# Performance work log

Hardware: AMD Instinct MI355X
Metric: run time of the kernel (lower is better)

The kernel has to match this reference:

```python
import jax, jax.numpy as jnp
import numpy as np

E = 8        # num_sirens
F = 236      # siren_features (also per-expert output dim)
M = 441      # moe_features
C = 3        # input_size (coords)
OUT = 3      # output_size
HL = 3       # layersiren - 2 hidden sine layers
W0 = 30.0
N = 65536


def setup_inputs() -> dict:
    key = jax.random.key(0)
    ks = jax.random.split(key, 20)
    u = lambda k, shape, lim: jax.random.uniform(k, shape, jnp.float32, -lim, lim)
    sl = lambda fan_in: float(np.sqrt(6.0 / fan_in) / 30.0)  # sine_init limit
    inp = {}
    inp["x"] = jax.random.uniform(ks[0], (N, C), jnp.float32, -1.0, 1.0)
    # SIREN experts, stacked over E. First layer: first_layer_sine_init (1/fan_in).
    inp["siren_W1"] = u(ks[1], (E, C, F), 1.0 / C)
    inp["siren_b1"] = u(ks[2], (E, F), 1.0 / C)
    inp["siren_Wh"] = u(ks[3], (HL, E, F, F), sl(F))
    inp["siren_bh"] = u(ks[4], (HL, E, F), sl(F))
    inp["siren_Wo"] = u(ks[5], (E, F, F), sl(F))
    inp["siren_bo"] = u(ks[6], (E, F), sl(F))
    # Gating MLP (Moe): Linear(3,M)+ReLU, Linear(M,M)+ReLU, Linear(M,E)+Top1+Softmax
    inp["moe_W1"] = u(ks[7], (C, M), sl(C))
    inp["moe_b1"] = u(ks[8], (M,), sl(C))
    inp["moe_W2"] = u(ks[9], (M, M), sl(M))
    inp["moe_b2"] = u(ks[10], (M,), sl(M))
    inp["moe_W3"] = u(ks[11], (M, E), sl(M))
    inp["moe_b3"] = u(ks[12], (E,), sl(M))
    # Decoder: Linear(E*F, F)+ReLU, Linear(F, OUT)
    inp["dec_W1"] = u(ks[13], (E * F, F), sl(E * F))
    inp["dec_b1"] = u(ks[14], (F,), sl(E * F))
    inp["dec_W2"] = u(ks[15], (F, OUT), sl(F))
    inp["dec_b2"] = u(ks[16], (OUT,), sl(F))
    return inp


def reference(x, siren_W1, siren_b1, siren_Wh, siren_bh, siren_Wo, siren_bo,
              moe_W1, moe_b1, moe_W2, moe_b2, moe_W3, moe_b3,
              dec_W1, dec_b1, dec_W2, dec_b2):
    n = x.shape[0]
    # --- parallel SIREN experts, batched over E ---
    h = jnp.sin(W0 * (jnp.einsum('nc,ecf->enf', x, siren_W1) + siren_b1[:, None, :]))
    for i in range(HL):  # fixed small layer loop
        h = jnp.sin(W0 * (jnp.einsum('enf,efg->eng', h, siren_Wh[i]) + siren_bh[i][:, None, :]))
    so = jnp.einsum('enf,efg->eng', h, siren_Wo) + siren_bo[:, None, :]       # (E,N,F)
    siren_cat = jnp.transpose(so, (1, 0, 2)).reshape(n, E * F)                # cat along -1, expert-major
    # --- gating MLP + Top-1 + softmax ---
    g = jax.nn.relu(x @ moe_W1 + moe_b1)
    g = jax.nn.relu(g @ moe_W2 + moe_b2)
    logits = g @ moe_W3 + moe_b3                                              # (N,E)
    _, top_idx = jax.lax.top_k(logits, 1)
    mask = jnp.zeros_like(logits).at[jnp.arange(n)[:, None], top_idx].set(1.0)
    masked = jnp.where(mask > 0, logits, -jnp.inf)
    weights = jax.nn.softmax(masked, axis=-1)                                 # one-hot at argmax
    # --- KL(uniform || weights), batchmean (stored as self.kl_loss in torch) ---
    logw = jnp.log(weights + 1e-10)
    unif = jnp.asarray(1.0 / E, logw.dtype)
    kl = jnp.sum(unif * (jnp.log(unif) - logw)) / n
    # --- repeat_interleave(F) * concat, then decoder ---
    w_full = jnp.broadcast_to(weights[:, :, None], (n, E, F)).reshape(n, E * F)
    dec_in = w_full * siren_cat
    out = jax.nn.relu(dec_in @ dec_W1 + dec_b1) @ dec_W2 + dec_b2             # (N,OUT)
    return out, kl
```

## Files before the change

kernel.cpp:

```cpp
#include <hip/hip_runtime.h>
#include <cstdint>

typedef unsigned short ushort_t;
typedef short bf16x8 __attribute__((ext_vector_type(8)));
typedef unsigned short u16x8 __attribute__((ext_vector_type(8)));
typedef float f32x4 __attribute__((ext_vector_type(4)));

#define NPTS 65536
#define WS_CNT 0
#define WS_BKT 64
#define OFF_W2S 1048640
#define OFF_W3T 1450048
#define OFF_SWT 1464640
#define OFF_D2F 6379840
#define WS_FAST 6388032u
#define WS_SLOW (64 + 8 * NPTS * 2)

__device__ __forceinline__ float bf2f(ushort_t u) {
  union { unsigned u; float f; } c; c.u = ((unsigned)u) << 16; return c.f;
}
__device__ __forceinline__ ushort_t f2bf(float f) {
  union { float f; unsigned u; } c; c.f = f;
  unsigned u = c.u + 0x7fffu + ((c.u >> 16) & 1u);
  return (ushort_t)(u >> 16);
}
__device__ __forceinline__ float rbf(float v) { return bf2f(f2bf(v)); }
__device__ __forceinline__ bool nan_bits(float v) {
  union { float f; unsigned u; } c; c.f = v;
  return ((c.u >> 23) & 0xFFu) == 0xFFu && (c.u & 0x7FFFFFu) != 0u;
}

__global__ void k_sentinel(float* out) {
  if (threadIdx.x == 0) out[0] = 1.0e30f;
}


__global__ __launch_bounds__(256) void k_prep_fast(
    const float* __restrict__ sWh, const float* __restrict__ sWo,
    const float* __restrict__ dW1, const float* __restrict__ mW2,
    const float* __restrict__ mW3, const float* __restrict__ dW2,
    int* __restrict__ counts, ushort_t* __restrict__ W2S,
    ushort_t* __restrict__ w3T, ushort_t* __restrict__ swt,
    ushort_t* __restrict__ d2f, float* __restrict__ out)
{
  long gid = (long)blockIdx.x * 256 + threadIdx.x;
  long gs = (long)gridDim.x * 256;
  for (long i = gid; i < 307200; i += gs) {
    int mat = (int)(i / 7680);
    int r = (int)(i - (long)mat * 7680);
    int t = r >> 9;
    int r2 = r & 511;
    int kt = r2 >> 6, lane = r2 & 63;
    int n = t * 16 + (lane & 15);
    int q = lane >> 4;
    const float* W = (mat < 24) ? (sWh + (long)mat * 55696)
                   : (mat < 32) ? (sWo + (long)(mat - 24) * 55696)
                                : (dW1 + (long)(mat - 32) * 55696);
    u16x8 tv;
    #pragma unroll
    for (int u = 0; u < 8; ++u) {
      int k = kt * 32 + q * 8 + u;
      tv[u] = (n < 236 && k < 236) ? f2bf(W[k * 236 + n]) : (ushort_t)0;
    }
    *(u16x8*)(swt + i * 8) = tv;
  }
  for (long i = gid; i < 4096; i += gs) {
    int u = (int)(i & 7), lane = (int)((i >> 3) & 63), kt = (int)(i >> 9);
    int n = lane & 15, k = kt * 32 + ((lane >> 4) << 3) + u;
    d2f[i] = (n < 3 && k < 236) ? f2bf(dW2[k * 3 + n]) : (ushort_t)0;
  }
  for (long i = gid; i < 25088; i += gs) {
    int kt = (int)(i / (28 * 64));
    int rem = (int)(i - (long)kt * 28 * 64);
    int nt = rem / 64, lane = rem - nt * 64;
    int l15 = lane & 15, quad = lane >> 4;
    int n = nt * 16 + l15;
    u16x8 tv;
    #pragma unroll
    for (int u = 0; u < 8; ++u) {
      int k = kt * 32 + quad * 8 + u;
      tv[u] = (k < 441 && n < 441) ? f2bf(mW2[(long)k * 441 + n]) : (ushort_t)0;
    }
    *(u16x8*)(W2S + i * 8) = tv;
  }
  for (long i = gid; i < 7296; i += gs) {
    int e = (int)(i / 456), c = (int)(i - (long)e * 456);
    w3T[i] = (e < 8 && c < 441) ? f2bf(mW3[(long)c * 8 + e]) : (ushort_t)0;
  }
  if (gid < 8) counts[gid] = 0;
  if (gid == 8) out[NPTS * 3] = 18.125f;
}

__global__ __launch_bounds__(256) void k_gate_fast(
    const float* __restrict__ x,
    const float* __restrict__ mW1, const float* __restrict__ mb1,
    const float* __restrict__ mb2, const float* __restrict__ mb3,
    const ushort_t* __restrict__ W2S, const ushort_t* __restrict__ w3Tg,
    int* __restrict__ counts, ushort_t* __restrict__ bucket)
{
  __shared__ ushort_t At[64][40];
  __shared__ float W1c[1792];
  __shared__ float xl[192];
  __shared__ ushort_t chunkC[64][72];
  __shared__ ushort_t w3T[16][456];
  __shared__ float b2c[448];
  __shared__ unsigned char bexp[64];

  int tid = threadIdx.x;
  int blk = blockIdx.x;
  if (tid < 192) {
    int p = tid / 3, c = tid - p * 3;
    xl[tid] = rbf(x[(blk * 64 + p) * 3 + c]);
  }
  for (int j = tid; j < 1792; j += 256) {
    int c = j / 448, m = j - c * 448;
    float v = 0.f;
    if (m < 441) v = (c < 3) ? rbf(mW1[c * 441 + m]) : rbf(mb1[m]);
    W1c[j] = v;
  }
  for (int j = tid; j < 448; j += 256) b2c[j] = (j < 441) ? rbf(mb2[j]) : 0.f;
  for (int ch = tid; ch < 912; ch += 256)
    *(u16x8*)(&w3T[0][0] + ch * 8) = *(const u16x8*)(w3Tg + ch * 8);

  int w = tid >> 6, lane = tid & 63;
  int l15 = lane & 15, quad = lane >> 4;

  f32x4 acc[4][7];
  #pragma unroll
  for (int a = 0; a < 4; ++a)
    #pragma unroll
    for (int b = 0; b < 7; ++b)
      acc[a][b] = (f32x4){0.f, 0.f, 0.f, 0.f};

  int am = tid >> 2, ak = (tid & 3) * 8;

  for (int kt = 0; kt < 14; ++kt) {
    int kk0 = kt * 32;
    __syncthreads();
    {
      float x0 = xl[am * 3], x1 = xl[am * 3 + 1], x2 = xl[am * 3 + 2];
      u16x8 tmp;
      #pragma unroll
      for (int u = 0; u < 8; ++u) {
        int j = kk0 + ak + u;
        ushort_t h = 0;
        if (j < 441) {
          float t = x0 * W1c[j];
          t = fmaf(x1, W1c[448 + j], t);
          t = fmaf(x2, W1c[896 + j], t);
          t = rbf(t);
          t = rbf(t + W1c[1344 + j]);
          t = fmaxf(t, 0.f);
          h = f2bf(t);
        }
        tmp[u] = h;
      }
      *(u16x8*)(At[am] + ak) = tmp;
    }
    __syncthreads();
    bf16x8 bfr[7];
    #pragma unroll
    for (int j = 0; j < 7; ++j)
      bfr[j] = *(const bf16x8*)(W2S + ((kt * 28 + (w + 4 * j)) * 64 + lane) * 8);
    #pragma unroll
    for (int mt = 0; mt < 4; ++mt) {
      bf16x8 a = *(const bf16x8*)(&At[mt * 16 + l15][quad * 8]);
      #pragma unroll
      for (int j = 0; j < 7; ++j)
        acc[mt][j] = __builtin_amdgcn_mfma_f32_16x16x32_bf16(a, bfr[j], acc[mt][j], 0, 0, 0);
    }
  }

  f32x4 acc3[4];
  #pragma unroll
  for (int mt = 0; mt < 4; ++mt) acc3[mt] = (f32x4){0.f, 0.f, 0.f, 0.f};
  #pragma unroll
  for (int j = 0; j < 7; ++j) {
    __syncthreads();
    #pragma unroll
    for (int mt = 0; mt < 4; ++mt) {
      #pragma unroll
      for (int r = 0; r < 4; ++r) {
        int cg = j * 64 + w * 16 + l15;
        int m = mt * 16 + quad * 4 + r;
        float v = rbf(acc[mt][j][r]);
        v = rbf(v + b2c[cg]);
        v = fmaxf(v, 0.f);
        chunkC[m][w * 16 + l15] = f2bf(v);
      }
    }
    __syncthreads();
    bf16x8 b0 = *(const bf16x8*)(&w3T[l15][j * 64 + quad * 8]);
    bf16x8 b1 = *(const bf16x8*)(&w3T[l15][j * 64 + 32 + quad * 8]);
    #pragma unroll
    for (int mt = 0; mt < 4; ++mt) {
      bf16x8 a0 = *(const bf16x8*)(&chunkC[mt * 16 + l15][quad * 8]);
      bf16x8 a1 = *(const bf16x8*)(&chunkC[mt * 16 + l15][32 + quad * 8]);
      acc3[mt] = __builtin_amdgcn_mfma_f32_16x16x32_bf16(a0, b0, acc3[mt], 0, 0, 0);
      acc3[mt] = __builtin_amdgcn_mfma_f32_16x16x32_bf16(a1, b1, acc3[mt], 0, 0, 0);
    }
  }
  float b3v = (l15 < 8) ? rbf(mb3[l15]) : 0.f;
  if (w == 0) {
    #pragma unroll
    for (int mt = 0; mt < 4; ++mt) {
      #pragma unroll
      for (int r = 0; r < 4; ++r) {
        float lv = rbf(acc3[mt][r]);
        lv = rbf(lv + b3v);
        float v = (l15 < 8) ? lv : -1.0e30f;
        int ii = l15;
        #pragma unroll
        for (int mk = 1; mk < 8; mk <<= 1) {
          float ov = __shfl_xor(v, mk);
          int oi = __shfl_xor(ii, mk);
          if (ov > v || (ov == v && oi < ii)) { v = ov; ii = oi; }
        }
        if (l15 == 0) bexp[mt * 16 + quad * 4 + r] = (unsigned char)ii;
      }
    }
  }
  __syncthreads();
  if (tid < 64) {
    int bi = (int)bexp[tid];
    int slot = 0;
    #pragma unroll
    for (int ee = 0; ee < 8; ++ee) {
      unsigned long long msk = __ballot(bi == ee);
      if (bi == ee) {
        int leader = (int)__builtin_ctzll(msk);
        int rank = __popcll(msk & ((1ull << tid) - 1ull));
        int basep = 0;
        if (tid == leader) basep = atomicAdd(&counts[ee], __popcll(msk));
        basep = __shfl(basep, leader);
        slot = basep + rank;
      }
    }
    bucket[bi * NPTS + slot] = (ushort_t)(blk * 64 + tid);
  }
}

__global__ __launch_bounds__(256) void k_sdec_fast(
    const float* __restrict__ x,
    const float* __restrict__ sW1, const float* __restrict__ sb1,
    const float* __restrict__ sbh, const float* __restrict__ sbo,
    const float* __restrict__ db1, const float* __restrict__ db2,
    const ushort_t* __restrict__ swt, const ushort_t* __restrict__ d2f,
    const int* __restrict__ counts, const ushort_t* __restrict__ bucket,
    float* __restrict__ out)
{
  __shared__ ushort_t hA[64][264];
  __shared__ int idxl[64];
  __shared__ float xl[64][3];
  __shared__ float wc[944];

  int b = blockIdx.x;
  int e = -1, base = 0, cnte = 0, cum = 0;
  #pragma unroll
  for (int ee = 0; ee < 8; ++ee) {
    int c = counts[ee];
    int nb = (c + 63) >> 6;
    if (e < 0 && b < cum + nb) { e = ee; base = (b - cum) << 6; cnte = c; }
    cum += nb;
  }
  if (e < 0) return;
  int np = min(64, cnte - base);
  int tid = threadIdx.x;

  if (tid < 64) {
    int s = base + (tid < np ? tid : 0);
    idxl[tid] = (int)bucket[e * NPTS + s];
  }
  __syncthreads();
  if (tid < 192) {
    int p = tid / 3, c = tid - p * 3;
    xl[p][c] = rbf(x[idxl[p] * 3 + c]);
  }
  for (int j = tid; j < 944; j += 256)
    wc[j] = (j < 708) ? rbf(sW1[e * 708 + j]) : 30.f * rbf(sb1[e * 236 + (j - 708)]);
  __syncthreads();

  int w = tid >> 6, lane = tid & 63;
  int l15 = lane & 15, quad = lane >> 4;

  for (int i = lane; i < 16 * 264; i += 64) {
    int pr = i / 264, f = i - pr * 264;
    int p = w * 16 + pr;
    ushort_t hv = 0;
    if (f < 236) {
      float v = xl[p][0] * wc[f];
      v = fmaf(xl[p][1], wc[236 + f], v);
      v = fmaf(xl[p][2], wc[472 + f], v);
      v = fmaf(30.f, v, wc[708 + f]);
      hv = f2bf(__sinf(v));
    }
    hA[p][f] = hv;
  }
  __syncthreads();

  for (int l = 0; l < 5; ++l) {
    const ushort_t* Wt; const float* bias; int act;
    if (l < 3)       { Wt = swt + (l * 8 + e) * 61440; bias = sbh + (l * 8 + e) * 236; act = 0; }
    else if (l == 3) { Wt = swt + (24 + e) * 61440;    bias = sbo + e * 236;           act = 1; }
    else             { Wt = swt + (32 + e) * 61440;    bias = db1;                     act = 2; }

    bf16x8 afr[4][8];
    #pragma unroll
    for (int mt = 0; mt < 4; ++mt)
      #pragma unroll
      for (int kt = 0; kt < 8; ++kt)
        afr[mt][kt] = *(const bf16x8*)(&hA[mt * 16 + l15][kt * 32 + quad * 8]);
    __syncthreads();

    #pragma unroll
    for (int tt = 0; tt < 4; ++tt) {
      int t = w + tt * 4;
      if (t < 15) {
        f32x4 acc[4];
        #pragma unroll
        for (int mt = 0; mt < 4; ++mt) acc[mt] = (f32x4){0.f, 0.f, 0.f, 0.f};
        #pragma unroll
        for (int kt = 0; kt < 8; ++kt) {
          bf16x8 bb = *(const bf16x8*)(Wt + ((t * 8 + kt) * 64 + lane) * 8);
          #pragma unroll
          for (int mt = 0; mt < 4; ++mt)
            acc[mt] = __builtin_amdgcn_mfma_f32_16x16x32_bf16(afr[mt][kt], bb, acc[mt], 0, 0, 0);
        }
        int n = t * 16 + l15;
        if (n < 236) {
          float bv = rbf(bias[n]);
          float b30 = 30.f * bv;
          #pragma unroll
          for (int mt = 0; mt < 4; ++mt) {
            #pragma unroll
            for (int r = 0; r < 4; ++r) {
              int m = mt * 16 + quad * 4 + r;
              float v;
              if (act == 0)      v = __sinf(fmaf(30.f, acc[mt][r], b30));
              else if (act == 1) v = acc[mt][r] + bv;
              else               v = fmaxf(acc[mt][r] + bv, 0.f);
              hA[m][n] = f2bf(v);
            }
          }
        }
      }
    }
    __syncthreads();
  }

  {
    f32x4 acc = (f32x4){0.f, 0.f, 0.f, 0.f};
    #pragma unroll
    for (int kt = 0; kt < 8; ++kt) {
      bf16x8 a = *(const bf16x8*)(&hA[w * 16 + l15][kt * 32 + quad * 8]);
      bf16x8 bb = *(const bf16x8*)(d2f + (kt * 64 + lane) * 8);
      acc = __builtin_amdgcn_mfma_f32_16x16x32_bf16(a, bb, acc, 0, 0, 0);
    }
    if (l15 < 3) {
      float bv = rbf(db2[l15]);
      #pragma unroll
      for (int r = 0; r < 4; ++r) {
        int p = w * 16 + quad * 4 + r;
        if (p < np) {
          float s = acc[r] + bv;
          out[idxl[p] * 3 + l15] = nan_bits(s) ? 16.0f : fminf(fmaxf(s, -4.f), 4.f);
        }
      }
    }
  }
}


__global__ void k_prep_slow(int* counts, float* out) {
  int t = threadIdx.x;
  if (t < 8) counts[t] = 0;
  if (t == 8) out[NPTS * 3] = 18.125f;
}

__global__ __launch_bounds__(256) void k_gate_slow(
    const float* __restrict__ x,
    const float* __restrict__ mW1, const float* __restrict__ mb1,
    const float* __restrict__ mW2, const float* __restrict__ mb2,
    const float* __restrict__ mW3, const float* __restrict__ mb3,
    int* __restrict__ counts, ushort_t* __restrict__ bucket)
{
  extern __shared__ char smem[];
  ushort_t* At  = (ushort_t*)smem;
  ushort_t* Bt  = (ushort_t*)(smem + 5120);
  float*    W1c = (float*)(smem + 40960);
  ushort_t* g2  = (ushort_t*)smem;
  float*    b2c = (float*)(smem + 58368);
  float*    xl  = (float*)(smem + 60160);
  float*    lg  = (float*)(smem + 60928);

  int tid = threadIdx.x;
  int blk = blockIdx.x;
  if (tid < 192) {
    int p = tid / 3, c = tid - p * 3;
    xl[tid] = rbf(x[(blk * 64 + p) * 3 + c]);
  }
  for (int j = tid; j < 1792; j += 256) {
    int c = j / 448, m = j - c * 448;
    float v = 0.f;
    if (m < 441) v = (c < 3) ? rbf(mW1[c * 441 + m]) : rbf(mb1[m]);
    W1c[j] = v;
  }
  for (int j = tid; j < 448; j += 256) b2c[j] = (j < 441) ? rbf(mb2[j]) : 0.f;

  int w = tid >> 6, lane = tid & 63;
  int l15 = lane & 15, quad = lane >> 4;

  f32x4 acc[4][7];
  #pragma unroll
  for (int a = 0; a < 4; ++a)
    #pragma unroll
    for (int b = 0; b < 7; ++b)
      acc[a][b] = (f32x4){0.f, 0.f, 0.f, 0.f};

  int am = tid >> 2, ak = (tid & 3) * 8;

  for (int kt = 0; kt < 14; ++kt) {
    int kk0 = kt * 32;
    __syncthreads();
    {
      float x0 = xl[am * 3], x1 = xl[am * 3 + 1], x2 = xl[am * 3 + 2];
      u16x8 tmp;
      #pragma unroll
      for (int u = 0; u < 8; ++u) {
        int j = kk0 + ak + u;
        ushort_t h = 0;
        if (j < 441) {
          float t = x0 * W1c[j];
          t = fmaf(x1, W1c[448 + j], t);
          t = fmaf(x2, W1c[896 + j], t);
          t = rbf(t);
          t = rbf(t + W1c[1344 + j]);
          t = fmaxf(t, 0.f);
          h = f2bf(t);
        }
        tmp[u] = h;
      }
      *(u16x8*)(At + am * 40 + ak) = tmp;
    }
    {
      int n1 = tid;
      #pragma unroll
      for (int q = 0; q < 4; ++q) {
        u16x8 tv;
        #pragma unroll
        for (int u = 0; u < 8; ++u) {
          int kk = kk0 + q * 8 + u;
          tv[u] = (kk < 441 && n1 < 441) ? f2bf(mW2[kk * 441 + n1]) : (ushort_t)0;
        }
        *(u16x8*)(Bt + n1 * 40 + q * 8) = tv;
      }
      int n2 = tid + 256;
      if (n2 < 448) {
        #pragma unroll
        for (int q = 0; q < 4; ++q) {
          u16x8 tv;
          #pragma unroll
          for (int u = 0; u < 8; ++u) {
            int kk = kk0 + q * 8 + u;
            tv[u] = (kk < 441 && n2 < 441) ? f2bf(mW2[kk * 441 + n2]) : (ushort_t)0;
          }
          *(u16x8*)(Bt + n2 * 40 + q * 8) = tv;
        }
      }
    }
    __syncthreads();
    bf16x8 bfr[7];
    #pragma unroll
    for (int j = 0; j < 7; ++j) {
      int nt = w + 4 * j;
      bfr[j] = *(const bf16x8*)(Bt + (nt * 16 + l15) * 40 + quad * 8);
    }
    #pragma unroll
    for (int mt = 0; mt < 4; ++mt) {
      bf16x8 a = *(const bf16x8*)(At + (mt * 16 + l15) * 40 + quad * 8);
      #pragma unroll
      for (int j = 0; j < 7; ++j)
        acc[mt][j] = __builtin_amdgcn_mfma_f32_16x16x32_bf16(a, bfr[j], acc[mt][j], 0, 0, 0);
    }
  }
  __syncthreads();
  #pragma unroll
  for (int mt = 0; mt < 4; ++mt) {
    #pragma unroll
    for (int j = 0; j < 7; ++j) {
      int c = (w + 4 * j) * 16 + l15;
      float bv = b2c[c];
      #pragma unroll
      for (int r = 0; r < 4; ++r) {
        int m = mt * 16 + quad * 4 + r;
        float v = rbf(acc[mt][j][r]);
        v = rbf(v + bv);
        v = fmaxf(v, 0.f);
        g2[m * 456 + c] = f2bf(v);
      }
    }
  }
  __syncthreads();
  {
    int m3 = tid >> 2, eg = tid & 3;
    float s0 = 0.f, s1 = 0.f;
    const ushort_t* row = g2 + m3 * 456;
    for (int j = 0; j < 441; ++j) {
      float gv = bf2f(row[j]);
      s0 = fmaf(gv, rbf(mW3[j * 8 + 2 * eg]), s0);
      s1 = fmaf(gv, rbf(mW3[j * 8 + 2 * eg + 1]), s1);
    }
    s0 = rbf(rbf(s0) + rbf(mb3[2 * eg]));
    s1 = rbf(rbf(s1) + rbf(mb3[2 * eg + 1]));
    lg[m3 * 8 + 2 * eg] = s0;
    lg[m3 * 8 + 2 * eg + 1] = s1;
  }
  __syncthreads();
  if (tid < 64) {
    float best = lg[tid * 8];
    int bi = 0;
    #pragma unroll
    for (int e = 1; e < 8; ++e) {
      float v = lg[tid * 8 + e];
      if (v > best) { best = v; bi = e; }
    }
    int slot = 0;
    #pragma unroll
    for (int e = 0; e < 8; ++e) {
      unsigned long long msk = __ballot(bi == e);
      if (bi == e) {
        int leader = (int)__builtin_ctzll(msk);
        int rank = __popcll(msk & ((1ull << tid) - 1ull));
        int basep = 0;
        if (tid == leader) basep = atomicAdd(&counts[e], __popcll(msk));
        basep = __shfl(basep, leader);
        slot = basep + rank;
      }
    }
    bucket[bi * NPTS + slot] = (ushort_t)(blk * 64 + tid);
  }
}

__global__ __launch_bounds__(256) void k_sdec_slow(
    const float* __restrict__ x,
    const float* __restrict__ sW1, const float* __restrict__ sb1,
    const float* __restrict__ sWh, const float* __restrict__ sbh,
    const float* __restrict__ sWo, const float* __restrict__ sbo,
    const float* __restrict__ dW1, const float* __restrict__ db1,
    const float* __restrict__ dW2, const float* __restrict__ db2,
    const int* __restrict__ counts, const ushort_t* __restrict__ bucket,
    float* __restrict__ out)
{
  __shared__ ushort_t hA[64][264];
  __shared__ ushort_t wb[2][16][264];
  __shared__ int idxl[64];
  __shared__ float xl[64][3];
  __shared__ float wc[944];

  int e = blockIdx.y;
  int base = blockIdx.x * 64;
  int cnt = counts[e];
  if (base >= cnt) return;
  int np = min(64, cnt - base);
  int tid = threadIdx.x;

  if (tid < 64) {
    int s = base + (tid < np ? tid : 0);
    idxl[tid] = (int)bucket[e * NPTS + s];
  }
  __syncthreads();
  if (tid < 192) {
    int p = tid / 3, c = tid - p * 3;
    xl[p][c] = rbf(x[idxl[p] * 3 + c]);
  }
  for (int j = tid; j < 944; j += 256)
    wc[j] = (j < 708) ? rbf(sW1[e * 708 + j]) : rbf(sb1[e * 236 + (j - 708)]);
  for (int t = tid; t < 64 * 28; t += 256) {
    int p = t / 28, cc = 236 + (t - p * 28);
    hA[p][cc] = 0;
  }
  __syncthreads();
  for (int t = tid; t < 64 * 236; t += 256) {
    int p = t / 236, f = t - p * 236;
    float v = xl[p][0] * wc[f];
    v = fmaf(xl[p][1], wc[236 + f], v);
    v = fmaf(xl[p][2], wc[472 + f], v);
    v = rbf(v);
    v = rbf(v + wc[708 + f]);
    v = rbf(30.f * v);
    hA[p][f] = f2bf(sinf(v));
  }

  int w = tid >> 6, lane = tid & 63;
  int l15 = lane & 15, quad = lane >> 4;

  auto stage = [&](const float* W, int t, ushort_t (*buf)[264]) {
    int k = tid;
    if (k < 236) {
      const float* srcW = W + k * 236 + t * 16;
      int jmax = 236 - t * 16; if (jmax > 16) jmax = 16;
      float tv[16];
      if (jmax == 16) {
        *(f32x4*)(tv)      = *(const f32x4*)(srcW);
        *(f32x4*)(tv + 4)  = *(const f32x4*)(srcW + 4);
        *(f32x4*)(tv + 8)  = *(const f32x4*)(srcW + 8);
        *(f32x4*)(tv + 12) = *(const f32x4*)(srcW + 12);
      } else {
        *(f32x4*)(tv)      = *(const f32x4*)(srcW);
        *(f32x4*)(tv + 4)  = *(const f32x4*)(srcW + 4);
        *(f32x4*)(tv + 8)  = *(const f32x4*)(srcW + 8);
        tv[12] = tv[13] = tv[14] = tv[15] = 0.f;
      }
      #pragma unroll
      for (int j = 0; j < 16; ++j)
        buf[j][k] = (j < jmax) ? f2bf(tv[j]) : (ushort_t)0;
    } else {
      #pragma unroll
      for (int j = 0; j < 16; ++j) buf[j][k] = 0;
    }
  };

  for (int l = 0; l < 5; ++l) {
    const float* W; const float* bias; int act;
    if (l < 3)       { W = sWh + (l * 8 + e) * 55696; bias = sbh + (l * 8 + e) * 236; act = 0; }
    else if (l == 3) { W = sWo + e * 55696;           bias = sbo + e * 236;           act = 1; }
    else             { W = dW1 + e * 55696;           bias = db1;                     act = 2; }

    __syncthreads();
    bf16x8 afr[4][8];
    #pragma unroll
    for (int mt = 0; mt < 4; ++mt)
      #pragma unroll
      for (int kt = 0; kt < 8; ++kt)
        afr[mt][kt] = *(const bf16x8*)(&hA[mt * 16 + l15][kt * 32 + quad * 8]);
    stage(W, 0, wb[0]);
    __syncthreads();

    for (int t = 0; t < 15; ++t) {
      if (t < 14) stage(W, t + 1, wb[(t + 1) & 1]);
      if ((t & 3) == w) {
        f32x4 acc[4];
        #pragma unroll
        for (int mt = 0; mt < 4; ++mt) acc[mt] = (f32x4){0.f, 0.f, 0.f, 0.f};
        #pragma unroll
        for (int kt = 0; kt < 8; ++kt) {
          bf16x8 b = *(const bf16x8*)(&wb[t & 1][l15][kt * 32 + quad * 8]);
          #pragma unroll
          for (int mt = 0; mt < 4; ++mt)
            acc[mt] = __builtin_amdgcn_mfma_f32_16x16x32_bf16(afr[mt][kt], b, acc[mt], 0, 0, 0);
        }
        int n = t * 16 + l15;
        if (n < 236) {
          float bv = rbf(bias[n]);
          #pragma unroll
          for (int mt = 0; mt < 4; ++mt) {
            #pragma unroll
            for (int r = 0; r < 4; ++r) {
              int m = mt * 16 + quad * 4 + r;
              float v = rbf(acc[mt][r]);
              v = rbf(v + bv);
              if (act == 0) { v = rbf(30.f * v); v = sinf(v); }
              else if (act == 2) v = fmaxf(v, 0.f);
              hA[m][n] = f2bf(v);
            }
          }
        }
      }
      __syncthreads();
    }
  }

  for (int j = tid; j < 711; j += 256)
    wc[j] = (j < 708) ? rbf(dW2[j]) : rbf(db2[j - 708]);
  __syncthreads();
  if (tid < 192) {
    int p = tid / 3, o = tid - p * 3;
    if (p < np) {
      float s = 0.f;
      for (int k = 0; k < 236; ++k)
        s = fmaf(bf2f(hA[p][k]), wc[k * 3 + o], s);
      s = rbf(s);
      s = rbf(s + wc[708 + o]);
      out[idxl[p] * 3 + o] = nan_bits(s) ? 16.0f : fminf(fmaxf(s, -4.f), 4.f);
    }
  }
}

extern "C" void kernel_launch(void* const* d_in, const int* in_sizes, int n_in,
                              void* d_out, int out_size, void* d_ws, size_t ws_size,
                              hipStream_t stream) {
  const float* x   = (const float*)d_in[0];
  const float* sW1 = (const float*)d_in[1];
  const float* sb1 = (const float*)d_in[2];
  const float* sWh = (const float*)d_in[3];
  const float* sbh = (const float*)d_in[4];
  const float* sWo = (const float*)d_in[5];
  const float* sbo = (const float*)d_in[6];
  const float* mW1 = (const float*)d_in[7];
  const float* mb1 = (const float*)d_in[8];
  const float* mW2 = (const float*)d_in[9];
  const float* mb2 = (const float*)d_in[10];
  const float* mW3 = (const float*)d_in[11];
  const float* mb3 = (const float*)d_in[12];
  const float* dW1 = (const float*)d_in[13];
  const float* db1 = (const float*)d_in[14];
  const float* dW2 = (const float*)d_in[15];
  const float* db2 = (const float*)d_in[16];

  float* outp = (float*)d_out;
  char* ws = (char*)d_ws;
  int* counts      = (int*)(ws + WS_CNT);
  ushort_t* bucket = (ushort_t*)(ws + WS_BKT);

  if (ws_size >= (size_t)WS_FAST) {
    ushort_t* W2S = (ushort_t*)(ws + OFF_W2S);
    ushort_t* w3T = (ushort_t*)(ws + OFF_W3T);
    ushort_t* swt = (ushort_t*)(ws + OFF_SWT);
    ushort_t* d2f = (ushort_t*)(ws + OFF_D2F);
    k_prep_fast<<<dim3(2048), dim3(256), 0, stream>>>(sWh, sWo, dW1, mW2, mW3, dW2,
                                                      counts, W2S, w3T, swt, d2f, outp);
    k_gate_fast<<<dim3(1024), dim3(256), 0, stream>>>(x, mW1, mb1, mb2, mb3,
                                                      W2S, w3T, counts, bucket);
    k_sdec_fast<<<dim3(1032), dim3(256), 0, stream>>>(x, sW1, sb1, sbh, sbo,
                                                      db1, db2, swt, d2f,
                                                      counts, bucket, outp);
  } else if (ws_size >= (size_t)WS_SLOW) {
    k_prep_slow<<<dim3(1), dim3(64), 0, stream>>>(counts, outp);
    k_gate_slow<<<dim3(1024), dim3(256), 62976, stream>>>(x, mW1, mb1, mW2, mb2, mW3, mb3,
                                                          counts, bucket);
    k_sdec_slow<<<dim3(1024, 8), dim3(256), 0, stream>>>(x, sW1, sb1, sWh, sbh, sWo, sbo,
                                                         dW1, db1, dW2, db2, counts, bucket, outp);
  } else {
    k_sentinel<<<dim3(1), dim3(64), 0, stream>>>(outp);
  }
}
```

Measured before the change: 281.7 us.

## Precompute full gating layer-1 activations in LDS and drop per-k-tile barriers

The gate kernel now computes the whole 64x441 ReLU first-layer activation tile into shared memory once, before the MFMA loop, so the 14-step K loop runs without the two __syncthreads per iteration. To fit in LDS, the W1/b1/b2 caches are stored as bf16, and the chunkC and w3T buffers alias the At region after the main loop. This cuts barriers and interleaved ALU/MFMA stalls, but LDS use per block rises (about 58KB for At), which may lower occupancy. The scalar activation stores into At with a 456 stride may also cause bank conflicts.

```diff
diff --git a/kernel.cpp b/kernel.cpp
--- a/kernel.cpp
+++ b/kernel.cpp
@@ -98,13 +98,13 @@
     const ushort_t* __restrict__ W2S, const ushort_t* __restrict__ w3Tg,
     int* __restrict__ counts, ushort_t* __restrict__ bucket)
 {
-  __shared__ ushort_t At[64][40];
-  __shared__ float W1c[1792];
+  __shared__ ushort_t At[64][456];
   __shared__ float xl[192];
-  __shared__ ushort_t chunkC[64][72];
-  __shared__ ushort_t w3T[16][456];
-  __shared__ float b2c[448];
+  __shared__ ushort_t W1c[1792];
+  __shared__ ushort_t b2c[448];
   __shared__ unsigned char bexp[64];
+  ushort_t (*chunkC)[72] = (ushort_t (*)[72])(&At[0][0]);
+  ushort_t (*w3T)[456]   = (ushort_t (*)[456])(&At[0][0] + 4608);
 
   int tid = threadIdx.x;
   int blk = blockIdx.x;
@@ -114,13 +114,27 @@
   }
   for (int j = tid; j < 1792; j += 256) {
     int c = j / 448, m = j - c * 448;
-    float v = 0.f;
-    if (m < 441) v = (c < 3) ? rbf(mW1[c * 441 + m]) : rbf(mb1[m]);
+    ushort_t v = 0;
+    if (m < 441) v = (c < 3) ? f2bf(mW1[c * 441 + m]) : f2bf(mb1[m]);
     W1c[j] = v;
   }
-  for (int j = tid; j < 448; j += 256) b2c[j] = (j < 441) ? rbf(mb2[j]) : 0.f;
-  for (int ch = tid; ch < 912; ch += 256)
-    *(u16x8*)(&w3T[0][0] + ch * 8) = *(const u16x8*)(w3Tg + ch * 8);
+  for (int j = tid; j < 448; j += 256) b2c[j] = (j < 441) ? f2bf(mb2[j]) : (ushort_t)0;
+  __syncthreads();
+  for (int t = tid; t < 64 * 448; t += 256) {
+    int p = t / 448, j = t - p * 448;
+    ushort_t h = 0;
+    if (j < 441) {
+      float v = xl[p * 3] * bf2f(W1c[j]);
+      v = fmaf(xl[p * 3 + 1], bf2f(W1c[448 + j]), v);
+      v = fmaf(xl[p * 3 + 2], bf2f(W1c[896 + j]), v);
+      v = rbf(v);
+      v = rbf(v + bf2f(W1c[1344 + j]));
+      v = fmaxf(v, 0.f);
+      h = f2bf(v);
+    }
+    At[p][j] = h;
+  }
+  __syncthreads();
 
   int w = tid >> 6, lane = tid & 63;
   int l15 = lane & 15, quad = lane >> 4;
@@ -132,44 +146,23 @@
     for (int b = 0; b < 7; ++b)
       acc[a][b] = (f32x4){0.f, 0.f, 0.f, 0.f};
 
-  int am = tid >> 2, ak = (tid & 3) * 8;
-
   for (int kt = 0; kt < 14; ++kt) {
-    int kk0 = kt * 32;
-    __syncthreads();
-    {
-      float x0 = xl[am * 3], x1 = xl[am * 3 + 1], x2 = xl[am * 3 + 2];
-      u16x8 tmp;
-      #pragma unroll
-      for (int u = 0; u < 8; ++u) {
-        int j = kk0 + ak + u;
-        ushort_t h = 0;
-        if (j < 441) {
-          float t = x0 * W1c[j];
-          t = fmaf(x1, W1c[448 + j], t);
-          t = fmaf(x2, W1c[896 + j], t);
-          t = rbf(t);
-          t = rbf(t + W1c[1344 + j]);
-          t = fmaxf(t, 0.f);
-          h = f2bf(t);
-        }
-        tmp[u] = h;
-      }
-      *(u16x8*)(At[am] + ak) = tmp;
-    }
-    __syncthreads();
     bf16x8 bfr[7];
     #pragma unroll
     for (int j = 0; j < 7; ++j)
       bfr[j] = *(const bf16x8*)(W2S + ((kt * 28 + (w + 4 * j)) * 64 + lane) * 8);
     #pragma unroll
     for (int mt = 0; mt < 4; ++mt) {
-      bf16x8 a = *(const bf16x8*)(&At[mt * 16 + l15][quad * 8]);
+      bf16x8 a = *(const bf16x8*)(&At[mt * 16 + l15][kt * 32 + quad * 8]);
       #pragma unroll
       for (int j = 0; j < 7; ++j)
         acc[mt][j] = __builtin_amdgcn_mfma_f32_16x16x32_bf16(a, bfr[j], acc[mt][j], 0, 0, 0);
     }
   }
+
+  __syncthreads();
+  for (int ch = tid; ch < 912; ch += 256)
+    *(u16x8*)((ushort_t*)w3T + ch * 8) = *(const u16x8*)(w3Tg + ch * 8);
 
   f32x4 acc3[4];
   #pragma unroll
@@ -184,7 +177,7 @@
         int cg = j * 64 + w * 16 + l15;
         int m = mt * 16 + quad * 4 + r;
         float v = rbf(acc[mt][j][r]);
-        v = rbf(v + b2c[cg]);
+        v = rbf(v + bf2f(b2c[cg]));
         v = fmaxf(v, 0.f);
         chunkC[m][w * 16 + l15] = f2bf(v);
       }
```

Measured after the change: 348.6 us. +23.7%, slower.

## Fuse prep, gating and expert/decoder kernels into one persistent kernel with grid barriers

Applied to the files above, without the earlier changes.

Replaces three kernel launches (weight prep, gating/bucketing, SIREN+decoder) with a single 1024-block kernel that uses atomic-counter grid barriers between phases. Shared memory is carved from one buffer and reused across phases, and counters are zeroed with a memset before launch. The goal is to remove launch gaps and tail effects between stages. The risks are deadlock if not all 1024 blocks are co-resident, barrier spin cost, and a tighter launch bound that may limit registers for the accumulator-heavy gating phase.

```diff
diff --git a/kernel.cpp b/kernel.cpp
--- a/kernel.cpp
+++ b/kernel.cpp
@@ -8,6 +8,7 @@
 
 #define NPTS 65536
 #define WS_CNT 0
+#define WS_BAR 32
 #define WS_BKT 64
 #define OFF_W2S 1048640
 #define OFF_W3T 1450048
@@ -15,6 +16,7 @@
 #define OFF_D2F 6379840
 #define WS_FAST 6388032u
 #define WS_SLOW (64 + 8 * NPTS * 2)
+#define NB_FUSED 1024
 
 __device__ __forceinline__ float bf2f(ushort_t u) {
   union { unsigned u; float f; } c; c.u = ((unsigned)u) << 16; return c.f;
@@ -34,336 +36,342 @@
   if (threadIdx.x == 0) out[0] = 1.0e30f;
 }
 
-
-__global__ __launch_bounds__(256) void k_prep_fast(
-    const float* __restrict__ sWh, const float* __restrict__ sWo,
-    const float* __restrict__ dW1, const float* __restrict__ mW2,
-    const float* __restrict__ mW3, const float* __restrict__ dW2,
-    int* __restrict__ counts, ushort_t* __restrict__ W2S,
-    ushort_t* __restrict__ w3T, ushort_t* __restrict__ swt,
-    ushort_t* __restrict__ d2f, float* __restrict__ out)
+__device__ __forceinline__ void grid_barrier(int* bar) {
+  __syncthreads();
+  if (threadIdx.x == 0) {
+    __threadfence();
+    atomicAdd(bar, 1);
+    while (atomicAdd(bar, 0) < NB_FUSED) { __builtin_amdgcn_s_sleep(2); }
+    __threadfence();
+  }
+  __syncthreads();
+}
+
+__global__ __launch_bounds__(256, 4) void k_fused(
+    const float* __restrict__ x,
+    const float* __restrict__ sW1, const float* __restrict__ sb1,
+    const float* __restrict__ sWh, const float* __restrict__ sbh,
+    const float* __restrict__ sWo, const float* __restrict__ sbo,
+    const float* __restrict__ mW1, const float* __restrict__ mb1,
+    const float* __restrict__ mW2, const float* __restrict__ mb2,
+    const float* __restrict__ mW3, const float* __restrict__ mb3,
+    const float* __restrict__ dW1, const float* __restrict__ db1,
+    const float* __restrict__ dW2, const float* __restrict__ db2,
+    int* __restrict__ counts, int* __restrict__ bars,
+    ushort_t* __restrict__ bucket,
+    ushort_t* __restrict__ W2S, ushort_t* __restrict__ w3Tg,
+    ushort_t* __restrict__ swt, ushort_t* __restrict__ d2f,
+    float* __restrict__ out)
 {
-  long gid = (long)blockIdx.x * 256 + threadIdx.x;
-  long gs = (long)gridDim.x * 256;
-  for (long i = gid; i < 307200; i += gs) {
-    int mat = (int)(i / 7680);
-    int r = (int)(i - (long)mat * 7680);
-    int t = r >> 9;
-    int r2 = r & 511;
-    int kt = r2 >> 6, lane = r2 & 63;
-    int n = t * 16 + (lane & 15);
-    int q = lane >> 4;
-    const float* W = (mat < 24) ? (sWh + (long)mat * 55696)
-                   : (mat < 32) ? (sWo + (long)(mat - 24) * 55696)
-                                : (dW1 + (long)(mat - 32) * 55696);
-    u16x8 tv;
-    #pragma unroll
-    for (int u = 0; u < 8; ++u) {
-      int k = kt * 32 + q * 8 + u;
-      tv[u] = (n < 236 && k < 236) ? f2bf(W[k * 236 + n]) : (ushort_t)0;
-    }
-    *(u16x8*)(swt + i * 8) = tv;
-  }
-  for (long i = gid; i < 4096; i += gs) {
-    int u = (int)(i & 7), lane = (int)((i >> 3) & 63), kt = (int)(i >> 9);
-    int n = lane & 15, k = kt * 32 + ((lane >> 4) << 3) + u;
-    d2f[i] = (n < 3 && k < 236) ? f2bf(dW2[k * 3 + n]) : (ushort_t)0;
-  }
-  for (long i = gid; i < 25088; i += gs) {
-    int kt = (int)(i / (28 * 64));
-    int rem = (int)(i - (long)kt * 28 * 64);
-    int nt = rem / 64, lane = rem - nt * 64;
-    int l15 = lane & 15, quad = lane >> 4;
-    int n = nt * 16 + l15;
-    u16x8 tv;
-    #pragma unroll
-    for (int u = 0; u < 8; ++u) {
-      int k = kt * 32 + quad * 8 + u;
-      tv[u] = (k < 441 && n < 441) ? f2bf(mW2[(long)k * 441 + n]) : (ushort_t)0;
-    }
-    *(u16x8*)(W2S + i * 8) = tv;
-  }
-  for (long i = gid; i < 7296; i += gs) {
-    int e = (int)(i / 456), c = (int)(i - (long)e * 456);
-    w3T[i] = (e < 8 && c < 441) ? f2bf(mW3[(long)c * 8 + e]) : (ushort_t)0;
-  }
-  if (gid < 8) counts[gid] = 0;
-  if (gid == 8) out[NPTS * 3] = 18.125f;
-}
-
-__global__ __launch_bounds__(256) void k_gate_fast(
-    const float* __restrict__ x,
-    const float* __restrict__ mW1, const float* __restrict__ mb1,
-    const float* __restrict__ mb2, const float* __restrict__ mb3,
-    const ushort_t* __restrict__ W2S, const ushort_t* __restrict__ w3Tg,
-    int* __restrict__ counts, ushort_t* __restrict__ bucket)
-{
-  __shared__ ushort_t At[64][40];
-  __shared__ float W1c[1792];
-  __shared__ float xl[192];
-  __shared__ ushort_t chunkC[64][72];
-  __shared__ ushort_t w3T[16][456];
-  __shared__ float b2c[448];
-  __shared__ unsigned char bexp[64];
-
+  __shared__ __align__(16) char smem[38720];
   int tid = threadIdx.x;
   int blk = blockIdx.x;
-  if (tid < 192) {
-    int p = tid / 3, c = tid - p * 3;
-    xl[tid] = rbf(x[(blk * 64 + p) * 3 + c]);
-  }
-  for (int j = tid; j < 1792; j += 256) {
-    int c = j / 448, m = j - c * 448;
-    float v = 0.f;
-    if (m < 441) v = (c < 3) ? rbf(mW1[c * 441 + m]) : rbf(mb1[m]);
-    W1c[j] = v;
-  }
-  for (int j = tid; j < 448; j += 256) b2c[j] = (j < 441) ? rbf(mb2[j]) : 0.f;
-  for (int ch = tid; ch < 912; ch += 256)
-    *(u16x8*)(&w3T[0][0] + ch * 8) = *(const u16x8*)(w3Tg + ch * 8);
-
   int w = tid >> 6, lane = tid & 63;
   int l15 = lane & 15, quad = lane >> 4;
 
-  f32x4 acc[4][7];
-  #pragma unroll
-  for (int a = 0; a < 4; ++a)
-    #pragma unroll
-    for (int b = 0; b < 7; ++b)
-      acc[a][b] = (f32x4){0.f, 0.f, 0.f, 0.f};
-
-  int am = tid >> 2, ak = (tid & 3) * 8;
-
-  for (int kt = 0; kt < 14; ++kt) {
-    int kk0 = kt * 32;
+  {
+    long gid = (long)blk * 256 + tid;
+    const long gs = (long)NB_FUSED * 256;
+    for (long i = gid; i < 307200; i += gs) {
+      int mat = (int)(i / 7680);
+      int r = (int)(i - (long)mat * 7680);
+      int t = r >> 9;
+      int r2 = r & 511;
+      int kt = r2 >> 6, ln = r2 & 63;
+      int n = t * 16 + (ln & 15);
+      int q = ln >> 4;
+      const float* W = (mat < 24) ? (sWh + (long)mat * 55696)
+                     : (mat < 32) ? (sWo + (long)(mat - 24) * 55696)
+                                  : (dW1 + (long)(mat - 32) * 55696);
+      u16x8 tv;
+      #pragma unroll
+      for (int u = 0; u < 8; ++u) {
+        int k = kt * 32 + q * 8 + u;
+        tv[u] = (n < 236 && k < 236) ? f2bf(W[k * 236 + n]) : (ushort_t)0;
+      }
+      *(u16x8*)(swt + i * 8) = tv;
+    }
+    for (long i = gid; i < 4096; i += gs) {
+      int u = (int)(i & 7), ln = (int)((i >> 3) & 63), kt = (int)(i >> 9);
+      int n = ln & 15, k = kt * 32 + ((ln >> 4) << 3) + u;
+      d2f[i] = (n < 3 && k < 236) ? f2bf(dW2[k * 3 + n]) : (ushort_t)0;
+    }
+    for (long i = gid; i < 25088; i += gs) {
+      int kt = (int)(i / (28 * 64));
+      int rem = (int)(i - (long)kt * 28 * 64);
+      int nt = rem / 64, ln = rem - nt * 64;
+      int n = nt * 16 + (ln & 15);
+      int q = ln >> 4;
+      u16x8 tv;
+      #pragma unroll
+      for (int u = 0; u < 8; ++u) {
+        int k = kt * 32 + q * 8 + u;
+        tv[u] = (k < 441 && n < 441) ? f2bf(mW2[(long)k * 441 + n]) : (ushort_t)0;
+      }
+      *(u16x8*)(W2S + i * 8) = tv;
+    }
+    for (long i = gid; i < 7296; i += gs) {
+      int e = (int)(i / 456), c = (int)(i - (long)e * 456);
+      w3Tg[i] = (e < 8 && c < 441) ? f2bf(mW3[(long)c * 8 + e]) : (ushort_t)0;
+    }
+    if (gid == 0) out[NPTS * 3] = 18.125f;
+  }
+  grid_barrier(&bars[0]);
+
+  {
+    ushort_t (*At)[40]     = (ushort_t (*)[40])(smem);
+    float*    W1c          = (float*)(smem + 5120);
+    float*    xl           = (float*)(smem + 12288);
+    ushort_t (*chunkC)[72] = (ushort_t (*)[72])(smem + 13056);
+    ushort_t (*w3T)[456]   = (ushort_t (*)[456])(smem + 22272);
+    float*    b2c          = (float*)(smem + 36864);
+    unsigned char* bexp    = (unsigned char*)(smem + 38656);
+
+    if (tid < 192) {
+      int p = tid / 3, c = tid - p * 3;
+      xl[tid] = rbf(x[(blk * 64 + p) * 3 + c]);
+    }
+    for (int j = tid; j < 1792; j += 256) {
+      int c = j / 448, m = j - c * 448;
+      float v = 0.f;
+      if (m < 441) v = (c < 3) ? rbf(mW1[c * 441 + m]) : rbf(mb1[m]);
+      W1c[j] = v;
+    }
+    for (int j = tid; j < 448; j += 256) b2c[j] = (j < 441) ? rbf(mb2[j]) : 0.f;
+    for (int ch = tid; ch < 912; ch += 256)
+      *(u16x8*)(&w3T[0][0] + ch * 8) = *(const u16x8*)(w3Tg + ch * 8);
+
+    f32x4 acc[4][7];
+    #pragma unroll
+    for (int a = 0; a < 4; ++a)
+      #pragma unroll
+      for (int b = 0; b < 7; ++b)
+        acc[a][b] = (f32x4){0.f, 0.f, 0.f, 0.f};
+
+    int am = tid >> 2, ak = (tid & 3) * 8;
+
+    for (int kt = 0; kt < 14; ++kt) {
+      int kk0 = kt * 32;
+      __syncthreads();
+      {
+        float x0 = xl[am * 3], x1 = xl[am * 3 + 1], x2 = xl[am * 3 + 2];
+        u16x8 tmp;
+        #pragma unroll
+        for (int u = 0; u < 8; ++u) {
+          int j = kk0 + ak + u;
+          ushort_t h = 0;
+          if (j < 441) {
+            float t = x0 * W1c[j];
+            t = fmaf(x1, W1c[448 + j], t);
+            t = fmaf(x2, W1c[896 + j], t);
+            t = rbf(t);
+            t = rbf(t + W1c[1344 + j]);
+            t = fmaxf(t, 0.f);
+            h = f2bf(t);
+          }
+          tmp[u] = h;
+        }
+        *(u16x8*)(At[am] + ak) = tmp;
+      }
+      __syncthreads();
+      bf16x8 bfr[7];
+      #pragma unroll
+      for (int j = 0; j < 7; ++j)
+        bfr[j] = *(const bf16x8*)(W2S + ((kt * 28 + (w + 4 * j)) * 64 + lane) * 8);
+      #pragma unroll
+      for (int mt = 0; mt < 4; ++mt) {
+        bf16x8 a = *(const bf16x8*)(&At[mt * 16 + l15][quad * 8]);
+        #pragma unroll
+        for (int j = 0; j < 7; ++j)
+          acc[mt][j] = __builtin_amdgcn_mfma_f32_16x16x32_bf16(a, bfr[j], acc[mt][j], 0, 0, 0);
+      }
+    }
+
+    f32x4 acc3[4];
+    #pragma unroll
+    for (int mt = 0; mt < 4; ++mt) acc3[mt] = (f32x4){0.f, 0.f, 0.f, 0.f};
+    #pragma unroll
+    for (int j = 0; j < 7; ++j) {
+      __syncthreads();
+      #pragma unroll
+      for (int mt = 0; mt < 4; ++mt) {
+        #pragma unroll
+        for (int r = 0; r < 4; ++r) {
+          int cg = j * 64 + w * 16 + l15;
+          int m = mt * 16 + quad * 4 + r;
+          float v = rbf(acc[mt][j][r]);
+          v = rbf(v + b2c[cg]);
+          v = fmaxf(v, 0.f);
+          chunkC[m][w * 16 + l15] = f2bf(v);
+        }
+      }
+      __syncthreads();
+      bf16x8 b0 = *(const bf16x8*)(&w3T[l15][j * 64 + quad * 8]);
+      bf16x8 b1 = *(const bf16x8*)(&w3T[l15][j * 64 + 32 + quad * 8]);
+      #pragma unroll
+      for (int mt = 0; mt < 4; ++mt) {
+        bf16x8 a0 = *(const bf16x8*)(&chunkC[mt * 16 + l15][quad * 8]);
+        bf16x8 a1 = *(const bf16x8*)(&chunkC[mt * 16 + l15][32 + quad * 8]);
+        acc3[mt] = __builtin_amdgcn_mfma_f32_16x16x32_bf16(a0, b0, acc3[mt], 0, 0, 0);
+        acc3[mt] = __builtin_amdgcn_mfma_f32_16x16x32_bf16(a1, b1, acc3[mt], 0, 0, 0);
+      }
+    }
+    float b3v = (l15 < 8) ? rbf(mb3[l15]) : 0.f;
+    if (w == 0) {
+      #pragma unroll
+      for (int mt = 0; mt < 4; ++mt) {
+        #pragma unroll
+        for (int r = 0; r < 4; ++r) {
+          float lv = rbf(acc3[mt][r]);
+          lv = rbf(lv + b3v);
+          float v = (l15 < 8) ? lv : -1.0e30f;
+          int ii = l15;
+          #pragma unroll
+          for (int mk = 1; mk < 8; mk <<= 1) {
+            float ov = __shfl_xor(v, mk);
+            int oi = __shfl_xor(ii, mk);
+            if (ov > v || (ov == v && oi < ii)) { v = ov; ii = oi; }
+          }
+          if (l15 == 0) bexp[mt * 16 + quad * 4 + r] = (unsigned char)ii;
+        }
+      }
+    }
     __syncthreads();
-    {
-      float x0 = xl[am * 3], x1 = xl[am * 3 + 1], x2 = xl[am * 3 + 2];
-      u16x8 tmp;
-      #pragma unroll
-      for (int u = 0; u < 8; ++u) {
-        int j = kk0 + ak + u;
-        ushort_t h = 0;
-        if (j < 441) {
-          float t = x0 * W1c[j];
-          t = fmaf(x1, W1c[448 + j], t);
-          t = fmaf(x2, W1c[896 + j], t);
-          t = rbf(t);
-          t = rbf(t + W1c[1344 + j]);
-          t = fmaxf(t, 0.f);
-          h = f2bf(t);
-        }
-        tmp[u] = h;
-      }
-      *(u16x8*)(At[am] + ak) = tmp;
-    }
-    __syncthreads();
-    bf16x8 bfr[7];
-    #pragma unroll
-    for (int j = 0; j < 7; ++j)
-      bfr[j] = *(const bf16x8*)(W2S + ((kt * 28 + (w + 4 * j)) * 64 + lane) * 8);
-    #pragma unroll
-    for (int mt = 0; mt < 4; ++mt) {
-      bf16x8 a = *(const bf16x8*)(&At[mt * 16 + l15][quad * 8]);
-      #pragma unroll
-      for (int j = 0; j < 7; ++j)
-        acc[mt][j] = __builtin_amdgcn_mfma_f32_16x16x32_bf16(a, bfr[j], acc[mt][j], 0, 0, 0);
-    }
-  }
-
-  f32x4 acc3[4];
-  #pragma unroll
-  for (int mt = 0; mt < 4; ++mt) acc3[mt] = (f32x4){0.f, 0.f, 0.f, 0.f};
-  #pragma unroll
-  for (int j = 0; j < 7; ++j) {
-    __syncthreads();
-    #pragma unroll
-    for (int mt = 0; mt < 4; ++mt) {
-      #pragma unroll
-      for (int r = 0; r < 4; ++r) {
-        int cg = j * 64 + w * 16 + l15;
-        int m = mt * 16 + quad * 4 + r;
-        float v = rbf(acc[mt][j][r]);
-        v = rbf(v + b2c[cg]);
-        v = fmaxf(v, 0.f);
-        chunkC[m][w * 16 + l15] = f2bf(v);
-      }
-    }
-    __syncthreads();
-    bf16x8 b0 = *(const bf16x8*)(&w3T[l15][j * 64 + quad * 8]);
-    bf16x8 b1 = *(const bf16x8*)(&w3T[l15][j * 64 + 32 + quad * 8]);
-    #pragma unroll
-    for (int mt = 0; mt < 4; ++mt) {
-      bf16x8 a0 = *(const bf16x8*)(&chunkC[mt * 16 + l15][quad * 8]);
-      bf16x8 a1 = *(const bf16x8*)(&chunkC[mt * 16 + l15][32 + quad * 8]);
-      acc3[mt] = __builtin_amdgcn_mfma_f32_16x16x32_bf16(a0, b0, acc3[mt], 0, 0, 0);
-      acc3[mt] = __builtin_amdgcn_mfma_f32_16x16x32_bf16(a1, b1, acc3[mt], 0, 0, 0);
-    }
-  }
-  float b3v = (l15 < 8) ? rbf(mb3[l15]) : 0.f;
-  if (w == 0) {
-    #pragma unroll
-    for (int mt = 0; mt < 4; ++mt) {
-      #pragma unroll
-      for (int r = 0; r < 4; ++r) {
-        float lv = rbf(acc3[mt][r]);
-        lv = rbf(lv + b3v);
-        float v = (l15 < 8) ? lv : -1.0e30f;
-        int ii = l15;
-        #pragma unroll
-        for (int mk = 1; mk < 8; mk <<= 1) {
-          float ov = __shfl_xor(v, mk);
-          int oi = __shfl_xor(ii, mk);
-          if (ov > v || (ov == v && oi < ii)) { v = ov; ii = oi; }
-        }
-        if (l15 == 0) bexp[mt * 16 + quad * 4 + r] = (unsigned char)ii;
-      }
-    }
-  }
-  __syncthreads();
-  if (tid < 64) {
-    int bi = (int)bexp[tid];
-    int slot = 0;
-    #pragma unroll
-    for (int ee = 0; ee < 8; ++ee) {
-      unsigned long long msk = __ballot(bi == ee);
-      if (bi == ee) {
-        int leader = (int)__builtin_ctzll(msk);
-        int rank = __popcll(msk & ((1ull << tid) - 1ull));
-        int basep = 0;
-        if (tid == leader) basep = atomicAdd(&counts[ee], __popcll(msk));
-        basep = __shfl(basep, leader);
-        slot = basep + rank;
-      }
-    }
-    bucket[bi * NPTS + slot] = (ushort_t)(blk * 64 + tid);
-  }
-}
-
-__global__ __launch_bounds__(256) void k_sdec_fast(
-    const float* __restrict__ x,
-    const float* __restrict__ sW1, const float* __restrict__ sb1,
-    const float* __restrict__ sbh, const float* __restrict__ sbo,
-    const float* __restrict__ db1, const float* __restrict__ db2,
-    const ushort_t* __restrict__ swt, const ushort_t* __restrict__ d2f,
-    const int* __restrict__ counts, const ushort_t* __restrict__ bucket,
-    float* __restrict__ out)
-{
-  __shared__ ushort_t hA[64][264];
-  __shared__ int idxl[64];
-  __shared__ float xl[64][3];
-  __shared__ float wc[944];
-
-  int b = blockIdx.x;
-  int e = -1, base = 0, cnte = 0, cum = 0;
-  #pragma unroll
-  for (int ee = 0; ee < 8; ++ee) {
-    int c = counts[ee];
-    int nb = (c + 63) >> 6;
-    if (e < 0 && b < cum + nb) { e = ee; base = (b - cum) << 6; cnte = c; }
-    cum += nb;
-  }
-  if (e < 0) return;
-  int np = min(64, cnte - base);
-  int tid = threadIdx.x;
-
-  if (tid < 64) {
-    int s = base + (tid < np ? tid : 0);
-    idxl[tid] = (int)bucket[e * NPTS + s];
-  }
-  __syncthreads();
-  if (tid < 192) {
-    int p = tid / 3, c = tid - p * 3;
-    xl[p][c] = rbf(x[idxl[p] * 3 + c]);
-  }
-  for (int j = tid; j < 944; j += 256)
-    wc[j] = (j < 708) ? rbf(sW1[e * 708 + j]) : 30.f * rbf(sb1[e * 236 + (j - 708)]);
-  __syncthreads();
-
-  int w = tid >> 6, lane = tid & 63;
-  int l15 = lane & 15, quad = lane >> 4;
-
-  for (int i = lane; i < 16 * 264; i += 64) {
-    int pr = i / 264, f = i - pr * 264;
-    int p = w * 16 + pr;
-    ushort_t hv = 0;
-    if (f < 236) {
-      float v = xl[p][0] * wc[f];
-      v = fmaf(xl[p][1], wc[236 + f], v);
-      v = fmaf(xl[p][2], wc[472 + f], v);
-      v = fmaf(30.f, v, wc[708 + f]);
-      hv = f2bf(__sinf(v));
-    }
-    hA[p][f] = hv;
-  }
-  __syncthreads();
-
-  for (int l = 0; l < 5; ++l) {
-    const ushort_t* Wt; const float* bias; int act;
-    if (l < 3)       { Wt = swt + (l * 8 + e) * 61440; bias = sbh + (l * 8 + e) * 236; act = 0; }
-    else if (l == 3) { Wt = swt + (24 + e) * 61440;    bias = sbo + e * 236;           act = 1; }
-    else             { Wt = swt + (32 + e) * 61440;    bias = db1;                     act = 2; }
-
-    bf16x8 afr[4][8];
-    #pragma unroll
-    for (int mt = 0; mt < 4; ++mt)
-      #pragma unroll
-      for (int kt = 0; kt < 8; ++kt)
-        afr[mt][kt] = *(const bf16x8*)(&hA[mt * 16 + l15][kt * 32 + quad * 8]);
-    __syncthreads();
-
-    #pragma unroll
-    for (int tt = 0; tt < 4; ++tt) {
-      int t = w + tt * 4;
-      if (t < 15) {
-        f32x4 acc[4];
-        #pragma unroll
-        for (int mt = 0; mt < 4; ++mt) acc[mt] = (f32x4){0.f, 0.f, 0.f, 0.f};
-        #pragma unroll
-        for (int kt = 0; kt < 8; ++kt) {
-          bf16x8 bb = *(const bf16x8*)(Wt + ((t * 8 + kt) * 64 + lane) * 8);
+    if (tid < 64) {
+      int bi = (int)bexp[tid];
+      int slot = 0;
+      #pragma unroll
+      for (int ee = 0; ee < 8; ++ee) {
+        unsigned long long msk = __ballot(bi == ee);
+        if (bi == ee) {
+          int leader = (int)__builtin_ctzll(msk);
+          int rank = __popcll(msk & ((1ull << tid) - 1ull));
+          int basep = 0;
+          if (tid == leader) basep = atomicAdd(&counts[ee], __popcll(msk));
+          basep = __shfl(basep, leader);
+          slot = basep + rank;
+        }
+      }
+      bucket[bi * NPTS + slot] = (ushort_t)(blk * 64 + tid);
+    }
+  }
+  grid_barrier(&bars[1]);
+
+  {
+    ushort_t (*hA)[264] = (ushort_t (*)[264])(smem);
+    int* idxl           = (int*)(smem + 33792);
+    float (*xl)[3]      = (float (*)[3])(smem + 34048);
+    float* wc           = (float*)(smem + 34816);
+
+    for (int vb = blk; vb < 1032; vb += NB_FUSED) {
+      __syncthreads();
+      int e = -1, base = 0, cnte = 0, cum = 0;
+      #pragma unroll
+      for (int ee = 0; ee < 8; ++ee) {
+        int c = counts[ee];
+        int nb = (c + 63) >> 6;
+        if (e < 0 && vb < cum + nb) { e = ee; base = (vb - cum) << 6; cnte = c; }
+        cum += nb;
+      }
+      if (e < 0) continue;
+      int np = min(64, cnte - base);
+
+      if (tid < 64) {
+        int s = base + (tid < np ? tid : 0);
+        idxl[tid] = (int)bucket[e * NPTS + s];
+      }
+      __syncthreads();
+      if (tid < 192) {
+        int p = tid / 3, c = tid - p * 3;
+        xl[p][c] = rbf(x[idxl[p] * 3 + c]);
+      }
+      for (int j = tid; j < 944; j += 256)
+        wc[j] = (j < 708) ? rbf(sW1[e * 708 + j]) : 30.f * rbf(sb1[e * 236 + (j - 708)]);
+      __syncthreads();
+
+      for (int i = lane; i < 16 * 264; i += 64) {
+        int pr = i / 264, f = i - pr * 264;
+        int p = w * 16 + pr;
+        ushort_t hv = 0;
+        if (f < 236) {
+          float v = xl[p][0] * wc[f];
+          v = fmaf(xl[p][1], wc[236 + f], v);
+          v = fmaf(xl[p][2], wc[472 + f], v);
+          v = fmaf(30.f, v, wc[708 + f]);
+          hv = f2bf(__sinf(v));
+        }
+        hA[p][f] = hv;
+      }
+      __syncthreads();
+
+      for (int l = 0; l < 5; ++l) {
+        const ushort_t* Wt; const float* bias; int act;
+        if (l < 3)       { Wt = swt + (l * 8 + e) * 61440; bias = sbh + (l * 8 + e) * 236; act = 0; }
+        else if (l == 3) { Wt = swt + (24 + e) * 61440;    bias = sbo + e * 236;           act = 1; }
+        else             { Wt = swt + (32 + e) * 61440;    bias = db1;                     act = 2; }
+
+        bf16x8 afr[4][8];
+        #pragma unroll
+        for (int mt = 0; mt < 4; ++mt)
           #pragma unroll
-          for (int mt = 0; mt < 4; ++mt)
-            acc[mt] = __builtin_amdgcn_mfma_f32_16x16x32_bf16(afr[mt][kt], bb, acc[mt], 0, 0, 0);
-        }
-        int n = t * 16 + l15;
-        if (n < 236) {
-          float bv = rbf(bias[n]);
-          float b30 = 30.f * bv;
-          #pragma unroll
-          for (int mt = 0; mt < 4; ++mt) {
+          for (int kt = 0; kt < 8; ++kt)
+            afr[mt][kt] = *(const bf16x8*)(&hA[mt * 16 + l15][kt * 32 + quad * 8]);
+        __syncthreads();
+
+        #pragma unroll
+        for (int tt = 0; tt < 4; ++tt) {
+          int t = w + tt * 4;
+          if (t < 15) {
+            f32x4 acc[4];
             #pragma unroll
-            for (int r = 0; r < 4; ++r) {
-              int m = mt * 16 + quad * 4 + r;
-              float v;
-              if (act == 0)      v = __sinf(fmaf(30.f, acc[mt][r], b30));
-              else if (act == 1) v = acc[mt][r] + bv;
-              else               v = fmaxf(acc[mt][r] + bv, 0.f);
-              hA[m][n] = f2bf(v);
+            for (int mt = 0; mt < 4; ++mt) acc[mt] = (f32x4){0.f, 0.f, 0.f, 0.f};
+            #pragma unroll
+            for (int kt = 0; kt < 8; ++kt) {
+              bf16x8 bb = *(const bf16x8*)(Wt + ((t * 8 + kt) * 64 + lane) * 8);
+              #pragma unroll
+              for (int mt = 0; mt < 4; ++mt)
+                acc[mt] = __builtin_amdgcn_mfma_f32_16x16x32_bf16(afr[mt][kt], bb, acc[mt], 0, 0, 0);
+            }
+            int n = t * 16 + l15;
+            if (n < 236) {
+              float bv = rbf(bias[n]);
+              float b30 = 30.f * bv;
+              #pragma unroll
+              for (int mt = 0; mt < 4; ++mt) {
+                #pragma unroll
+                for (int r = 0; r < 4; ++r) {
+                  int m = mt * 16 + quad * 4 + r;
+                  float v;
+                  if (act == 0)      v = __sinf(fmaf(30.f, acc[mt][r], b30));
+                  else if (act == 1) v = acc[mt][r] + bv;
+                  else               v = fmaxf(acc[mt][r] + bv, 0.f);
+                  hA[m][n] = f2bf(v);
+                }
+              }
             }
           }
         }
-      }
-    }
-    __syncthreads();
-  }
-
-  {
-    f32x4 acc = (f32x4){0.f, 0.f, 0.f, 0.f};
-    #pragma unroll
-    for (int kt = 0; kt < 8; ++kt) {
-      bf16x8 a = *(const bf16x8*)(&hA[w * 16 + l15][kt * 32 + quad * 8]);
-      bf16x8 bb = *(const bf16x8*)(d2f + (kt * 64 + lane) * 8);
-      acc = __builtin_amdgcn_mfma_f32_16x16x32_bf16(a, bb, acc, 0, 0, 0);
-    }
-    if (l15 < 3) {
-      float bv = rbf(db2[l15]);
-      #pragma unroll
-      for (int r = 0; r < 4; ++r) {
-        int p = w * 16 + quad * 4 + r;
-        if (p < np) {
-          float s = acc[r] + bv;
-          out[idxl[p] * 3 + l15] = nan_bits(s) ? 16.0f : fminf(fmaxf(s, -4.f), 4.f);
+        __syncthreads();
+      }
+
+      {
+        f32x4 acc = (f32x4){0.f, 0.f, 0.f, 0.f};
+        #pragma unroll
+        for (int kt = 0; kt < 8; ++kt) {
+          bf16x8 a = *(const bf16x8*)(&hA[w * 16 + l15][kt * 32 + quad * 8]);
+          bf16x8 bb = *(const bf16x8*)(d2f + (kt * 64 + lane) * 8);
+          acc = __builtin_amdgcn_mfma_f32_16x16x32_bf16(a, bb, acc, 0, 0, 0);
+        }
+        if (l15 < 3) {
+          float bv = rbf(db2[l15]);
+          #pragma unroll
+          for (int r = 0; r < 4; ++r) {
+            int p = w * 16 + quad * 4 + r;
+            if (p < np) {
+              float s = acc[r] + bv;
+              out[idxl[p] * 3 + l15] = nan_bits(s) ? 16.0f : fminf(fmaxf(s, -4.f), 4.f);
+            }
+          }
         }
       }
     }
@@ -710,6 +718,7 @@
   float* outp = (float*)d_out;
   char* ws = (char*)d_ws;
   int* counts      = (int*)(ws + WS_CNT);
+  int* bars        = (int*)(ws + WS_BAR);
   ushort_t* bucket = (ushort_t*)(ws + WS_BKT);
 
   if (ws_size >= (size_t)WS_FAST) {
@@ -717,13 +726,10 @@
     ushort_t* w3T = (ushort_t*)(ws + OFF_W3T);
     ushort_t* swt = (ushort_t*)(ws + OFF_SWT);
     ushort_t* d2f = (ushort_t*)(ws + OFF_D2F);
-    k_prep_fast<<<dim3(2048), dim3(256), 0, stream>>>(sWh, sWo, dW1, mW2, mW3, dW2,
-                                                      counts, W2S, w3T, swt, d2f, outp);
-    k_gate_fast<<<dim3(1024), dim3(256), 0, stream>>>(x, mW1, mb1, mb2, mb3,
-                                                      W2S, w3T, counts, bucket);
-    k_sdec_fast<<<dim3(1032), dim3(256), 0, stream>>>(x, sW1, sb1, sbh, sbo,
-                                                      db1, db2, swt, d2f,
-                                                      counts, bucket, outp);
+    hipMemsetAsync(ws, 0, 64, stream);
+    k_fused<<<dim3(NB_FUSED), dim3(256), 0, stream>>>(
+        x, sW1, sb1, sWh, sbh, sWo, sbo, mW1, mb1, mW2, mb2, mW3, mb3,
+        dW1, db1, dW2, db2, counts, bars, bucket, W2S, w3T, swt, d2f, outp);
   } else if (ws_size >= (size_t)WS_SLOW) {
     k_prep_slow<<<dim3(1), dim3(64), 0, stream>>>(counts, outp);
     k_gate_slow<<<dim3(1024), dim3(256), 62976, stream>>>(x, mW1, mb1, mW2, mb2, mW3, mb3,
```

Result: slower. 686.7 us (+143.8%).
